# Optimization experiments

Hardware: AMD Instinct MI355X
Metric: run time of the kernel (lower is better)

## Reference

```python
import jax, jax.numpy as jnp
import numpy as np

I, O, R = 64, 64, 896          # input / output / regulatory protein counts
N = I + O + R                  # total GRN size
WARMUP = 25                    # warmup_count


def setup_inputs() -> dict:
    key = jax.random.key(0)
    k1, k2, k3, k4 = jax.random.split(key, 4)
    return {
        "inputs": jax.random.uniform(k1, (16384, I), dtype=jnp.float32),
        "identifiers": jax.random.uniform(k2, (N,), dtype=jnp.float32),
        "enhancers": jax.random.uniform(k3, (N,), dtype=jnp.float32),
        "inhibitors": jax.random.uniform(k4, (N,), dtype=jnp.float32),
        "beta": jnp.full((1,), 2.0, dtype=jnp.float32),
        "delta": jnp.full((1,), 1.0, dtype=jnp.float32),
    }


def _signatures(identifiers, enhancers, inhibitors, beta):
    # sig[j, i] = exp(-beta * |tag_j - id_i|): affinity of protein j regulating protein i.
    enh = jnp.exp(-beta * jnp.abs(enhancers[:, None] - identifiers[None, :]))
    inh = jnp.exp(-beta * jnp.abs(inhibitors[:, None] - identifiers[None, :]))
    # output proteins do not regulate others -> zero their rows
    mask = jnp.ones((N,), dtype=enh.dtype).at[I:I + O].set(0.0)[:, None]
    return enh * mask, inh * mask


def _step(conc, sig_diff, delta):
    # conc: [..., N]; sig_diff = enh_sigs - inh_sigs: [N, N]
    dc = (delta / N) * (conc @ sig_diff)
    new = jnp.maximum(conc + dc, 0.0)
    reg = new[..., I:]                                    # outputs + regulatory
    s = jnp.sum(reg, axis=-1, keepdims=True)
    reg = jnp.where(s > 0, reg / s, reg)                  # renormalize
    return jnp.concatenate([conc[..., :I], reg], axis=-1)  # inputs clamped


def reference(inputs, identifiers, enhancers, inhibitors, beta, delta):
    b, d = beta[0], delta[0]
    enh_s, inh_s = _signatures(identifiers, enhancers, inhibitors, b)
    sig_diff = enh_s - inh_s

    # setup(): uniform initial concentrations; warmup(): shared sequential steps
    conc0 = jnp.full((N,), 1.0 / N, dtype=jnp.float32)
    def warm(c, _):
        return _step(c, sig_diff, d), None
    conc, _ = jax.lax.scan(warm, conc0, None, length=WARMUP)

    # per-sample (batched instead of tf.map_fn): set input concs, one step
    B = inputs.shape[0]
    batch_conc = jnp.concatenate(
        [inputs, jnp.broadcast_to(conc[I:], (B, N - I))], axis=-1)
    new = _step(batch_conc, sig_diff, d)
    return new[..., I:I + O]  # output protein concentrations [B, O]
```

## Files before the change

kernel.cpp:

```cpp
#include <hip/hip_runtime.h>
#include <math.h>

#define NJ 960
#define NSRC 896
#define NWARM 25

typedef unsigned long long u64;
typedef unsigned int u32;

#define RK_O 0u
#define CT_O 896u
#define HD_O 1856u
#define BASE_F 8192u

#define TAG_RK 0x524B0001u
#define TAG_CT 0x43540001u
#define TAG_HD 0x48440001u

__device__ __forceinline__ void ast(u64* p, u64 v) {
  __hip_atomic_store(p, v, __ATOMIC_RELAXED, __HIP_MEMORY_SCOPE_AGENT);
}
__device__ __forceinline__ u64 ald(const u64* p) {
  return __hip_atomic_load(p, __ATOMIC_RELAXED, __HIP_MEMORY_SCOPE_AGENT);
}
__device__ __forceinline__ u32 poll32(const u64* p, u32 tag) {
  u64 v = ald(p);
  while ((u32)(v >> 32) != tag) { __builtin_amdgcn_s_sleep(1); v = ald(p); }
  return (u32)v;
}

__global__ __launch_bounds__(256) void front_k(const float* __restrict__ ident,
                                               const float* __restrict__ enh,
                                               const float* __restrict__ inh,
                                               const float* __restrict__ beta,
                                               const float* __restrict__ delta,
                                               void* __restrict__ wsv) {
  u64* RK = (u64*)wsv + RK_O;
  u64* CT = (u64*)wsv + CT_O;
  u64* HD = (u64*)wsv + HD_O;
  float* base = (float*)wsv + BASE_F;

  const int tid = threadIdx.x;
  const float bb = beta[0];
  const float dN = delta[0] / 1024.0f;

  if (blockIdx.x > 0) {
    const int g = (int)(blockIdx.x - 1) * 256 + tid;
    const int c8 = g & 7;
    if (g < NSRC * 8) {
      int m = g >> 3;
      float myE = enh[128 + m], myI = inh[128 + m];
      int re = 0, ri = 0;
      for (int i = 112 * c8; i < 112 * c8 + 112; ++i) {
        float ev = enh[128 + i], iv = inh[128 + i];
        re += (ev < myE || (ev == myE && i < m)) ? 1 : 0;
        ri += (iv < myI || (iv == myI && i < m)) ? 1 : 0;
      }
      int p = re | (ri << 16);
      p += __shfl_xor(p, 1); p += __shfl_xor(p, 2); p += __shfl_xor(p, 4);
      if (c8 == 0) ast(&RK[m], ((u64)TAG_RK << 32) | (u32)p);
    }
    {
      int j = g >> 3;
      float cj = ident[64 + j];
      int ce = 0, ci = 0;
      for (int i = 112 * c8; i < 112 * c8 + 112; ++i) {
        ce += (enh[128 + i] <= cj) ? 1 : 0;
        ci += (inh[128 + i] <= cj) ? 1 : 0;
      }
      int p = ce | (ci << 16);
      p += __shfl_xor(p, 1); p += __shfl_xor(p, 2); p += __shfl_xor(p, 4);
      if (c8 == 0) ast(&CT[j], ((u64)TAG_CT << 32) | (u32)p);
    }
    {
      int j = g >> 3;
      float cj = ident[64 + j];
      float h = 0.0f;
      for (int k = 8 * c8; k < 8 * c8 + 8; ++k)
        h += expf(-bb * fabsf(enh[k] - cj)) - expf(-bb * fabsf(inh[k] - cj));
      h += __shfl_xor(h, 1); h += __shfl_xor(h, 2); h += __shfl_xor(h, 4);
      if (c8 == 0)
        ast(&HD[j], ((u64)TAG_HD << 32) |
                    (u64)__float_as_uint(dN * h * (1.0f / 1024.0f)));
    }
    return;
  }

  __shared__ float yl[NJ];
  __shared__ float2 scanE[1024];
  __shared__ float2 scanI[1024];
  __shared__ float4 wtot[4];
  __shared__ float ssw[4];

  const int lane = tid & 63, wvid = tid >> 6;

  int rE[4], rI[4];
  if (tid < 224) {
    #pragma unroll
    for (int s = 0; s < 4; ++s) {
      u32 v = poll32(&RK[4 * tid + s], TAG_RK);
      rE[s] = v & 0xFFFF; rI[s] = v >> 16;
    }
  }
  int cE[4], cI[4];
  float hd[4], fm[4], fp[4];
  if (tid < 240) {
    #pragma unroll
    for (int c = 0; c < 4; ++c) {
      u32 v = poll32(&CT[4 * tid + c], TAG_CT);
      cE[c] = v & 0xFFFF; cI[c] = v >> 16;
      hd[c] = __uint_as_float(poll32(&HD[4 * tid + c], TAG_HD));
      float cj = ident[64 + 4 * tid + c];
      fm[c] = expf(-bb * cj); fp[c] = expf(bb * cj);
    }
  }
  float EP[4], EN[4], IP[4], IN2[4];
  if (tid < 224) {
    #pragma unroll
    for (int s = 0; s < 4; ++s) {
      float e = enh[128 + 4 * tid + s], i2 = inh[128 + 4 * tid + s];
      EP[s] = expf(bb * e);  EN[s] = expf(-bb * e);
      IP[s] = expf(bb * i2); IN2[s] = expf(-bb * i2);
    }
  }
  float y_own[4] = {1.0f / 1024.0f, 1.0f / 1024.0f, 1.0f / 1024.0f, 1.0f / 1024.0f};
  if (tid < 240) {
    #pragma unroll
    for (int c = 0; c < 4; ++c) yl[4 * tid + c] = 1.0f / 1024.0f;
  }
  __syncthreads();

  for (int t = 0; t <= NWARM; ++t) {
    if (tid == 0) {
      scanE[0] = make_float2(0.f, 0.f);
      scanI[0] = make_float2(0.f, 0.f);
    }
    if (tid >= 224) {
      #pragma unroll
      for (int c = 0; c < 4; ++c) {
        int p = 4 * tid + c;
        if (p > NSRC) {
          scanE[p] = make_float2(0.f, 0.f);
          scanI[p] = make_float2(0.f, 0.f);
        }
      }
    }
    if (tid < 224) {
      #pragma unroll
      for (int s = 0; s < 4; ++s) {
        float ym = yl[64 + 4 * tid + s];
        scanE[rE[s] + 1] = make_float2(ym * EP[s], ym * EN[s]);
        scanI[rI[s] + 1] = make_float2(ym * IP[s], ym * IN2[s]);
      }
    }
    __syncthreads();

    float2 e0 = scanE[4 * tid], e1 = scanE[4 * tid + 1],
           e2 = scanE[4 * tid + 2], e3 = scanE[4 * tid + 3];
    float2 i0 = scanI[4 * tid], i1 = scanI[4 * tid + 1],
           i2v = scanI[4 * tid + 2], i3 = scanI[4 * tid + 3];
    e1.x += e0.x; e1.y += e0.y; e2.x += e1.x; e2.y += e1.y; e3.x += e2.x; e3.y += e2.y;
    i1.x += i0.x; i1.y += i0.y; i2v.x += i1.x; i2v.y += i1.y; i3.x += i2v.x; i3.y += i2v.y;
    float4 tot = make_float4(e3.x, e3.y, i3.x, i3.y);
    float4 inc = tot;
    #pragma unroll
    for (int off = 1; off < 64; off <<= 1) {
      float ox = __shfl_up(inc.x, off, 64);
      float oy = __shfl_up(inc.y, off, 64);
      float oz = __shfl_up(inc.z, off, 64);
      float ow = __shfl_up(inc.w, off, 64);
      if (lane >= off) { inc.x += ox; inc.y += oy; inc.z += oz; inc.w += ow; }
    }
    if (lane == 63) wtot[wvid] = inc;
    __syncthreads();
    float4 exc = make_float4(inc.x - tot.x, inc.y - tot.y,
                             inc.z - tot.z, inc.w - tot.w);
    #pragma unroll
    for (int w = 0; w < 3; ++w)
      if (w < wvid) {
        float4 p = wtot[w];
        exc.x += p.x; exc.y += p.y; exc.z += p.z; exc.w += p.w;
      }
    e0.x += exc.x; e0.y += exc.y; e1.x += exc.x; e1.y += exc.y;
    e2.x += exc.x; e2.y += exc.y; e3.x += exc.x; e3.y += exc.y;
    i0.x += exc.z; i0.y += exc.w; i1.x += exc.z; i1.y += exc.w;
    i2v.x += exc.z; i2v.y += exc.w; i3.x += exc.z; i3.y += exc.w;
    scanE[4 * tid] = e0; scanE[4 * tid + 1] = e1;
    scanE[4 * tid + 2] = e2; scanE[4 * tid + 3] = e3;
    scanI[4 * tid] = i0; scanI[4 * tid + 1] = i1;
    scanI[4 * tid + 2] = i2v; scanI[4 * tid + 3] = i3;
    __syncthreads();

    float nv[4] = {0.f, 0.f, 0.f, 0.f};
    float psum = 0.0f;
    if (tid < 240) {
      float2 TE = scanE[NSRC], TI = scanI[NSRC];
      #pragma unroll
      for (int c = 0; c < 4; ++c) {
        float2 AE = scanE[cE[c]], AI = scanI[cI[c]];
        float dot = fm[c] * AE.x + fp[c] * (TE.y - AE.y)
                  - fm[c] * AI.x - fp[c] * (TI.y - AI.y);
        float pre = y_own[c] + dN * dot;
        if (t < NWARM) {
          nv[c] = fmaxf(pre + hd[c], 0.0f);
          psum += nv[c];
        } else {
          base[4 * tid + c] = pre;
        }
      }
    }
    if (t < NWARM) {
      #pragma unroll
      for (int off = 32; off >= 1; off >>= 1) psum += __shfl_xor(psum, off);
      if (lane == 0) ssw[wvid] = psum;
      __syncthreads();
      float s = ssw[0] + ssw[1] + ssw[2] + ssw[3];
      float inv = (s > 0.0f) ? 1.0f / s : 1.0f;
      if (tid < 240) {
        #pragma unroll
        for (int c = 0; c < 4; ++c) {
          y_own[c] = nv[c] * inv;
          yl[4 * tid + c] = y_own[c];
        }
      }
    }
    __syncthreads();
  }
}

__global__ __launch_bounds__(512) void batch_k(const float* __restrict__ inp,
                                               const float* __restrict__ ident,
                                               const float* __restrict__ enh,
                                               const float* __restrict__ inh,
                                               const float* __restrict__ beta,
                                               const float* __restrict__ delta,
                                               const float* __restrict__ ws,
                                               float* __restrict__ out) {
  __shared__ float At[64][66];
  __shared__ float Wl[16][512];
  __shared__ float bch[NJ];
  __shared__ float4 Ek4[64];
  __shared__ float2 Ei2[64];

  const int tid = threadIdx.x;
  const int colg = tid & 63;
  const int rowg = tid >> 6;
  const size_t rowbase = (size_t)blockIdx.x * 64;
  const float bb = beta[0];
  const float dN = delta[0] / 1024.0f;

  #pragma unroll
  for (int i = 0; i < 2; ++i) {
    int fi = tid + i * 512;
    int r = fi >> 4, c4 = (fi & 15) * 4;
    float4 f4 = *(const float4*)(inp + (rowbase + r) * 64 + c4);
    At[c4 + 0][r] = f4.x; At[c4 + 1][r] = f4.y;
    At[c4 + 2][r] = f4.z; At[c4 + 3][r] = f4.w;
  }
  if (tid < 64) {
    float e = enh[tid], iv = inh[tid];
    Ek4[tid] = make_float4(expf(bb * e), expf(-bb * e),
                           expf(bb * iv), expf(-bb * iv));
    Ei2[tid] = make_float2(e, iv);
  }
  if (tid < 240) {
    float4 b4 = *(const float4*)(ws + BASE_F + 4 * tid);
    bch[4 * tid + 0] = b4.x; bch[4 * tid + 1] = b4.y;
    bch[4 * tid + 2] = b4.z; bch[4 * tid + 3] = b4.w;
  }

  float acc[8][8];
  float rs[8];
  #pragma unroll
  for (int r = 0; r < 8; ++r) rs[r] = 0.0f;

  #pragma unroll 1
  for (int ch = 0; ch < 2; ++ch) {
    const int c0 = ch ? 0 : 512;
    const bool ok = (c0 + tid) < NJ;
    const float cj = ok ? ident[64 + c0 + tid] : 0.0f;
    const float fpc = expf(bb * cj), fmc = expf(-bb * cj);

    #pragma unroll
    for (int r = 0; r < 8; ++r)
      #pragma unroll
      for (int c = 0; c < 8; ++c) acc[r][c] = 0.0f;

    #pragma unroll 1
    for (int s = 0; s < 4; ++s) {
      __syncthreads();
      #pragma unroll 4
      for (int e = 0; e < 16; ++e) {
        int k = 16 * s + e;
        float4 E = Ek4[k];
        float2 ei = Ei2[k];
        float w = 0.0f;
        if (ok)
          w = dN * (((ei.x >= cj) ? E.y * fpc : E.x * fmc)
                  - ((ei.y >= cj) ? E.w * fpc : E.z * fmc));
        Wl[e][tid] = w;
      }
      __syncthreads();
      #pragma unroll
      for (int kk = 0; kk < 16; ++kk) {
        float4 a0 = *(const float4*)&At[16 * s + kk][rowg * 8];
        float4 a1 = *(const float4*)&At[16 * s + kk][rowg * 8 + 4];
        float4 w0 = *(const float4*)&Wl[kk][colg * 4];
        float4 w1 = *(const float4*)&Wl[kk][256 + colg * 4];
        float a_[8] = {a0.x, a0.y, a0.z, a0.w, a1.x, a1.y, a1.z, a1.w};
        float w_[8] = {w0.x, w0.y, w0.z, w0.w, w1.x, w1.y, w1.z, w1.w};
        #pragma unroll
        for (int r = 0; r < 8; ++r)
          #pragma unroll
          for (int c = 0; c < 8; ++c)
            acc[r][c] = fmaf(a_[r], w_[c], acc[r][c]);
      }
    }

    #pragma unroll
    for (int c = 0; c < 8; ++c) {
      int cl = (c < 4) ? (colg * 4 + c) : (256 + colg * 4 + (c - 4));
      int j = c0 + cl;
      float bv = (j < NJ) ? bch[j] : -1.0e30f;
      #pragma unroll
      for (int r = 0; r < 8; ++r)
        rs[r] += fmaxf(acc[r][c] + bv, 0.0f);
    }
  }

  #pragma unroll
  for (int r = 0; r < 8; ++r) {
    float v = rs[r];
    #pragma unroll
    for (int off = 32; off >= 1; off >>= 1) v += __shfl_xor(v, off);
    rs[r] = v;
  }
  if (colg < 16) {
    #pragma unroll
    for (int r = 0; r < 8; ++r) {
      float inv = (rs[r] > 0.0f) ? 1.0f / rs[r] : 1.0f;
      float* op = out + (rowbase + rowg * 8 + r) * 64 + colg * 4;
      float4 o;
      o.x = fmaxf(acc[r][0] + bch[colg * 4 + 0], 0.0f) * inv;
      o.y = fmaxf(acc[r][1] + bch[colg * 4 + 1], 0.0f) * inv;
      o.z = fmaxf(acc[r][2] + bch[colg * 4 + 2], 0.0f) * inv;
      o.w = fmaxf(acc[r][3] + bch[colg * 4 + 3], 0.0f) * inv;
      *(float4*)op = o;
    }
  }
}

extern "C" void kernel_launch(void* const* d_in, const int* in_sizes, int n_in,
                              void* d_out, int out_size, void* d_ws, size_t ws_size,
                              hipStream_t stream) {
  const float* inp   = (const float*)d_in[0];
  const float* ident = (const float*)d_in[1];
  const float* enh   = (const float*)d_in[2];
  const float* inh   = (const float*)d_in[3];
  const float* beta  = (const float*)d_in[4];
  const float* delta = (const float*)d_in[5];

  hipLaunchKernelGGL(front_k, dim3(31), dim3(256), 0, stream,
                     ident, enh, inh, beta, delta, d_ws);
  hipLaunchKernelGGL(batch_k, dim3(256), dim3(512), 0, stream,
                     inp, ident, enh, inh, beta, delta,
                     (const float*)d_ws, (float*)d_out);
}
```

Baseline: 160.8 us.

## Precompute input-row weight matrix in front kernel and halve batch tile rows

The 64x960 input-to-node weight block is now computed once by 30 extra blocks in the front kernel and stored in the workspace. The batch kernel streams these weights from global memory instead of recomputing exponentials per block. The batch tile also shrinks from 64 to 32 rows, which doubles the grid to 512 blocks for better occupancy and CU coverage. In exchange, each block has a lower FMA-to-load ratio and extra global weight traffic, which L2 should mostly serve.

```diff
diff --git a/kernel.cpp b/kernel.cpp
--- a/kernel.cpp
+++ b/kernel.cpp
@@ -11,7 +11,8 @@
 #define RK_O 0u
 #define CT_O 896u
 #define HD_O 1856u
-#define BASE_F 8192u
+#define WK_F 8192u
+#define BASE_F 69632u
 
 #define TAG_RK 0x524B0001u
 #define TAG_CT 0x43540001u
@@ -38,11 +39,26 @@
   u64* RK = (u64*)wsv + RK_O;
   u64* CT = (u64*)wsv + CT_O;
   u64* HD = (u64*)wsv + HD_O;
+  float* Wk = (float*)wsv + WK_F;
   float* base = (float*)wsv + BASE_F;
 
   const int tid = threadIdx.x;
   const float bb = beta[0];
   const float dN = delta[0] / 1024.0f;
+
+  if (blockIdx.x > 30) {
+    const int g2 = (int)(blockIdx.x - 31) * 256 + tid;
+    int k = g2 / 120;
+    int jb = (g2 % 120) * 8;
+    float ek = enh[k], ik = inh[k];
+    #pragma unroll
+    for (int u = 0; u < 8; ++u) {
+      float cj = ident[64 + jb + u];
+      Wk[(size_t)k * NJ + jb + u] =
+          dN * (expf(-bb * fabsf(ek - cj)) - expf(-bb * fabsf(ik - cj)));
+    }
+    return;
+  }
 
   if (blockIdx.x > 0) {
     const int g = (int)(blockIdx.x - 1) * 256 + tid;
@@ -229,39 +245,23 @@
 }
 
 __global__ __launch_bounds__(512) void batch_k(const float* __restrict__ inp,
-                                               const float* __restrict__ ident,
-                                               const float* __restrict__ enh,
-                                               const float* __restrict__ inh,
-                                               const float* __restrict__ beta,
-                                               const float* __restrict__ delta,
                                                const float* __restrict__ ws,
                                                float* __restrict__ out) {
-  __shared__ float At[64][66];
+  __shared__ float At[64][36];
   __shared__ float Wl[16][512];
   __shared__ float bch[NJ];
-  __shared__ float4 Ek4[64];
-  __shared__ float2 Ei2[64];
 
   const int tid = threadIdx.x;
   const int colg = tid & 63;
   const int rowg = tid >> 6;
-  const size_t rowbase = (size_t)blockIdx.x * 64;
-  const float bb = beta[0];
-  const float dN = delta[0] / 1024.0f;
-
-  #pragma unroll
-  for (int i = 0; i < 2; ++i) {
-    int fi = tid + i * 512;
-    int r = fi >> 4, c4 = (fi & 15) * 4;
+  const size_t rowbase = (size_t)blockIdx.x * 32;
+  const float* __restrict__ Wk = ws + WK_F;
+
+  {
+    int r = tid >> 4, c4 = (tid & 15) * 4;
     float4 f4 = *(const float4*)(inp + (rowbase + r) * 64 + c4);
     At[c4 + 0][r] = f4.x; At[c4 + 1][r] = f4.y;
     At[c4 + 2][r] = f4.z; At[c4 + 3][r] = f4.w;
-  }
-  if (tid < 64) {
-    float e = enh[tid], iv = inh[tid];
-    Ek4[tid] = make_float4(expf(bb * e), expf(-bb * e),
-                           expf(bb * iv), expf(-bb * iv));
-    Ei2[tid] = make_float2(e, iv);
   }
   if (tid < 240) {
     float4 b4 = *(const float4*)(ws + BASE_F + 4 * tid);
@@ -269,48 +269,42 @@
     bch[4 * tid + 2] = b4.z; bch[4 * tid + 3] = b4.w;
   }
 
-  float acc[8][8];
-  float rs[8];
-  #pragma unroll
-  for (int r = 0; r < 8; ++r) rs[r] = 0.0f;
+  float acc[4][8];
+  float rs[4] = {0.f, 0.f, 0.f, 0.f};
 
   #pragma unroll 1
   for (int ch = 0; ch < 2; ++ch) {
     const int c0 = ch ? 0 : 512;
-    const bool ok = (c0 + tid) < NJ;
-    const float cj = ok ? ident[64 + c0 + tid] : 0.0f;
-    const float fpc = expf(bb * cj), fmc = expf(-bb * cj);
-
-    #pragma unroll
-    for (int r = 0; r < 8; ++r)
+
+    #pragma unroll
+    for (int r = 0; r < 4; ++r)
       #pragma unroll
       for (int c = 0; c < 8; ++c) acc[r][c] = 0.0f;
 
     #pragma unroll 1
     for (int s = 0; s < 4; ++s) {
       __syncthreads();
-      #pragma unroll 4
-      for (int e = 0; e < 16; ++e) {
-        int k = 16 * s + e;
-        float4 E = Ek4[k];
-        float2 ei = Ei2[k];
-        float w = 0.0f;
-        if (ok)
-          w = dN * (((ei.x >= cj) ? E.y * fpc : E.x * fmc)
-                  - ((ei.y >= cj) ? E.w * fpc : E.z * fmc));
-        Wl[e][tid] = w;
+      #pragma unroll
+      for (int i = 0; i < 4; ++i) {
+        int fi = tid + i * 512;
+        int kk = fi >> 7;
+        int c4 = (fi & 127) * 4;
+        int j = c0 + c4;
+        float4 v = make_float4(0.f, 0.f, 0.f, 0.f);
+        if (j < NJ)
+          v = *(const float4*)(Wk + (size_t)(16 * s + kk) * NJ + j);
+        *(float4*)&Wl[kk][c4] = v;
       }
       __syncthreads();
       #pragma unroll
       for (int kk = 0; kk < 16; ++kk) {
-        float4 a0 = *(const float4*)&At[16 * s + kk][rowg * 8];
-        float4 a1 = *(const float4*)&At[16 * s + kk][rowg * 8 + 4];
+        float4 av = *(const float4*)&At[16 * s + kk][rowg * 4];
         float4 w0 = *(const float4*)&Wl[kk][colg * 4];
         float4 w1 = *(const float4*)&Wl[kk][256 + colg * 4];
-        float a_[8] = {a0.x, a0.y, a0.z, a0.w, a1.x, a1.y, a1.z, a1.w};
+        float a_[4] = {av.x, av.y, av.z, av.w};
         float w_[8] = {w0.x, w0.y, w0.z, w0.w, w1.x, w1.y, w1.z, w1.w};
         #pragma unroll
-        for (int r = 0; r < 8; ++r)
+        for (int r = 0; r < 4; ++r)
           #pragma unroll
           for (int c = 0; c < 8; ++c)
             acc[r][c] = fmaf(a_[r], w_[c], acc[r][c]);
@@ -323,13 +317,13 @@
       int j = c0 + cl;
       float bv = (j < NJ) ? bch[j] : -1.0e30f;
       #pragma unroll
-      for (int r = 0; r < 8; ++r)
+      for (int r = 0; r < 4; ++r)
         rs[r] += fmaxf(acc[r][c] + bv, 0.0f);
     }
   }
 
   #pragma unroll
-  for (int r = 0; r < 8; ++r) {
+  for (int r = 0; r < 4; ++r) {
     float v = rs[r];
     #pragma unroll
     for (int off = 32; off >= 1; off >>= 1) v += __shfl_xor(v, off);
@@ -337,9 +331,9 @@
   }
   if (colg < 16) {
     #pragma unroll
-    for (int r = 0; r < 8; ++r) {
+    for (int r = 0; r < 4; ++r) {
       float inv = (rs[r] > 0.0f) ? 1.0f / rs[r] : 1.0f;
-      float* op = out + (rowbase + rowg * 8 + r) * 64 + colg * 4;
+      float* op = out + (rowbase + rowg * 4 + r) * 64 + colg * 4;
       float4 o;
       o.x = fmaxf(acc[r][0] + bch[colg * 4 + 0], 0.0f) * inv;
       o.y = fmaxf(acc[r][1] + bch[colg * 4 + 1], 0.0f) * inv;
@@ -360,9 +354,8 @@
   const float* beta  = (const float*)d_in[4];
   const float* delta = (const float*)d_in[5];
 
-  hipLaunchKernelGGL(front_k, dim3(31), dim3(256), 0, stream,
+  hipLaunchKernelGGL(front_k, dim3(61), dim3(256), 0, stream,
                      ident, enh, inh, beta, delta, d_ws);
-  hipLaunchKernelGGL(batch_k, dim3(256), dim3(512), 0, stream,
-                     inp, ident, enh, inh, beta, delta,
-                     (const float*)d_ws, (float*)d_out);
-}
+  hipLaunchKernelGGL(batch_k, dim3(512), dim3(512), 0, stream,
+                     inp, (const float*)d_ws, (float*)d_out);
+}
```

Measured after the change: 155.1 us. -3.6%, faster.

## Fuse warmup and batch kernels, overlapping per-block warmup scan with GEMM

Applied to the files above, without the earlier changes.

Merges the two-kernel pipeline into one 576-thread kernel. Every block redundantly runs the 25-step warmup recurrence in a dedicated high-priority wave using a single-wave scan, while 8 other waves compute the batch GEMM chunks that do not need the warmup bias. An LDS flag signals when the bias is ready, and the first chunk is computed after that. This removes the second launch and the global round trip for the bias, at the cost of redundant warmup work in all 256 blocks and inter-block polling on the tagged counters.

```diff
diff --git a/kernel.cpp b/kernel.cpp
--- a/kernel.cpp
+++ b/kernel.cpp
@@ -11,7 +11,6 @@
 #define RK_O 0u
 #define CT_O 896u
 #define HD_O 1856u
-#define BASE_F 8192u
 
 #define TAG_RK 0x524B0001u
 #define TAG_CT 0x43540001u
@@ -25,27 +24,58 @@
 }
 __device__ __forceinline__ u32 poll32(const u64* p, u32 tag) {
   u64 v = ald(p);
-  while ((u32)(v >> 32) != tag) { __builtin_amdgcn_s_sleep(1); v = ald(p); }
+  while ((u32)(v >> 32) != tag) { __builtin_amdgcn_s_sleep(8); v = ald(p); }
   return (u32)v;
 }
 
-__global__ __launch_bounds__(256) void front_k(const float* __restrict__ ident,
-                                               const float* __restrict__ enh,
-                                               const float* __restrict__ inh,
-                                               const float* __restrict__ beta,
-                                               const float* __restrict__ delta,
-                                               void* __restrict__ wsv) {
+__global__ __launch_bounds__(576) void grn_one(
+    const float* __restrict__ inp, const float* __restrict__ ident,
+    const float* __restrict__ enh, const float* __restrict__ inh,
+    const float* __restrict__ beta, const float* __restrict__ delta,
+    void* __restrict__ wsv, float* __restrict__ out) {
+  __shared__ float2 SE[16][64];
+  __shared__ float2 SI[16][64];
+  __shared__ float4 SRCX[NSRC];
+  __shared__ float4 HEK[64];
+  __shared__ float2 HEI[64];
+  __shared__ float At[64][68];
+  __shared__ float bch[NJ];
+  __shared__ u32 sflag;
+
   u64* RK = (u64*)wsv + RK_O;
   u64* CT = (u64*)wsv + CT_O;
   u64* HD = (u64*)wsv + HD_O;
-  float* base = (float*)wsv + BASE_F;
 
   const int tid = threadIdx.x;
   const float bb = beta[0];
   const float dN = delta[0] / 1024.0f;
-
-  if (blockIdx.x > 0) {
-    const int g = (int)(blockIdx.x - 1) * 256 + tid;
+  const size_t rowbase = (size_t)blockIdx.x * 64;
+
+  #pragma unroll
+  for (int it = 0; it < 2; ++it) {
+    int fi = tid + it * 576;
+    if (fi < 1024) {
+      int r = fi >> 4, c4 = (fi & 15) * 4;
+      float4 f4 = *(const float4*)(inp + (rowbase + r) * 64 + c4);
+      At[c4 + 0][r] = f4.x; At[c4 + 1][r] = f4.y;
+      At[c4 + 2][r] = f4.z; At[c4 + 3][r] = f4.w;
+    }
+  }
+  for (int m = tid; m < NSRC; m += 576) {
+    float e = enh[128 + m], iv = inh[128 + m];
+    SRCX[m] = make_float4(expf(bb * e), expf(-bb * e),
+                          expf(bb * iv), expf(-bb * iv));
+  }
+  if (tid < 64) {
+    float e = enh[tid], iv = inh[tid];
+    HEK[tid] = make_float4(expf(bb * e), expf(-bb * e),
+                           expf(bb * iv), expf(-bb * iv));
+    HEI[tid] = make_float2(e, iv);
+  }
+  if (tid == 0) sflag = 0;
+
+  if (blockIdx.x < 30 && tid < 256) {
+    const int g = (int)blockIdx.x * 256 + tid;
     const int c8 = g & 7;
     if (g < NSRC * 8) {
       int m = g >> 3;
@@ -83,250 +113,186 @@
         ast(&HD[j], ((u64)TAG_HD << 32) |
                     (u64)__float_as_uint(dN * h * (1.0f / 1024.0f)));
     }
+  }
+  __syncthreads();
+
+  if (tid >= 512) {
+    __builtin_amdgcn_s_setprio(1);
+    const int lane = tid - 512;
+    const int c0l = lane * 15;
+
+    #pragma unroll
+    for (int u = 0; u < 16; ++u) {
+      SE[u][lane] = make_float2(0.f, 0.f);
+      SI[u][lane] = make_float2(0.f, 0.f);
+    }
+
+    float fmv[15], fpv[15], hdv[15], y[15];
+    int cc[15], rr[15];
+    #pragma unroll
+    for (int s = 0; s < 15; ++s) {
+      float cj = ident[64 + c0l + s];
+      fmv[s] = expf(-bb * cj); fpv[s] = expf(bb * cj);
+      y[s] = 1.0f / 1024.0f;
+      rr[s] = 0;
+    }
+    #pragma unroll
+    for (int s = 0; s < 15; ++s) {
+      cc[s] = (int)poll32(&CT[c0l + s], TAG_CT);
+      hdv[s] = __uint_as_float(poll32(&HD[c0l + s], TAG_HD));
+    }
+    #pragma unroll
+    for (int s = 0; s < 15; ++s) {
+      int c = c0l + s;
+      if (c >= 64) rr[s] = (int)poll32(&RK[c - 64], TAG_RK);
+    }
+
+    for (int t = 0; t <= NWARM; ++t) {
+      #pragma unroll
+      for (int s = 0; s < 15; ++s) {
+        int c = c0l + s;
+        if (c >= 64) {
+          float4 X = SRCX[c - 64];
+          int qE = (rr[s] & 0xFFFF) + 1;
+          int qI = ((rr[s] >> 16) & 0xFFFF) + 1;
+          SE[qE & 15][qE >> 4] = make_float2(y[s] * X.x, y[s] * X.y);
+          SI[qI & 15][qI >> 4] = make_float2(y[s] * X.z, y[s] * X.w);
+        }
+      }
+      asm volatile("s_waitcnt lgkmcnt(0)" ::: "memory");
+      __builtin_amdgcn_sched_barrier(0);
+
+      float2 tE = make_float2(0.f, 0.f), tI = make_float2(0.f, 0.f);
+      #pragma unroll
+      for (int u = 0; u < 16; ++u) {
+        float2 a = SE[u][lane], b = SI[u][lane];
+        tE.x += a.x; tE.y += a.y; tI.x += b.x; tI.y += b.y;
+      }
+      float4 inc = make_float4(tE.x, tE.y, tI.x, tI.y);
+      float4 tot = inc;
+      #pragma unroll
+      for (int off = 1; off < 64; off <<= 1) {
+        float ox = __shfl_up(inc.x, off, 64);
+        float oy = __shfl_up(inc.y, off, 64);
+        float oz = __shfl_up(inc.z, off, 64);
+        float ow = __shfl_up(inc.w, off, 64);
+        if (lane >= off) { inc.x += ox; inc.y += oy; inc.z += oz; inc.w += ow; }
+      }
+      float TEy = __shfl(inc.y, 63, 64);
+      float TIy = __shfl(inc.w, 63, 64);
+      float2 pe = make_float2(inc.x - tot.x, inc.y - tot.y);
+      float2 pi = make_float2(inc.z - tot.z, inc.w - tot.w);
+
+      #pragma unroll
+      for (int u = 0; u < 16; ++u) {
+        float2 a = SE[u][lane], b = SI[u][lane];
+        pe.x += a.x; pe.y += a.y; pi.x += b.x; pi.y += b.y;
+        if (lane * 16 + u <= NSRC) { SE[u][lane] = pe; SI[u][lane] = pi; }
+      }
+      asm volatile("s_waitcnt lgkmcnt(0)" ::: "memory");
+      __builtin_amdgcn_sched_barrier(0);
+
+      float nv[15]; float psum = 0.0f;
+      #pragma unroll
+      for (int s = 0; s < 15; ++s) {
+        int cE = cc[s] & 0xFFFF, cI = (cc[s] >> 16) & 0xFFFF;
+        float2 AE = SE[cE & 15][cE >> 4];
+        float2 AI = SI[cI & 15][cI >> 4];
+        float dot = fmv[s] * AE.x + fpv[s] * (TEy - AE.y)
+                  - fmv[s] * AI.x - fpv[s] * (TIy - AI.y);
+        float pre = y[s] + dN * dot;
+        if (t < NWARM) {
+          nv[s] = fmaxf(pre + hdv[s], 0.0f);
+          psum += nv[s];
+        } else {
+          bch[c0l + s] = pre;
+        }
+      }
+      if (t < NWARM) {
+        #pragma unroll
+        for (int off = 32; off >= 1; off >>= 1) psum += __shfl_xor(psum, off);
+        float invs = (psum > 0.0f) ? 1.0f / psum : 1.0f;
+        #pragma unroll
+        for (int s = 0; s < 15; ++s) y[s] = nv[s] * invs;
+      }
+    }
+    asm volatile("s_waitcnt lgkmcnt(0)" ::: "memory");
+    __hip_atomic_store(&sflag, 1u, __ATOMIC_RELEASE,
+                       __HIP_MEMORY_SCOPE_WORKGROUP);
+    __builtin_amdgcn_s_setprio(0);
     return;
   }
 
-  __shared__ float yl[NJ];
-  __shared__ float2 scanE[1024];
-  __shared__ float2 scanI[1024];
-  __shared__ float4 wtot[4];
-  __shared__ float ssw[4];
-
-  const int lane = tid & 63, wvid = tid >> 6;
-
-  int rE[4], rI[4];
-  if (tid < 224) {
-    #pragma unroll
-    for (int s = 0; s < 4; ++s) {
-      u32 v = poll32(&RK[4 * tid + s], TAG_RK);
-      rE[s] = v & 0xFFFF; rI[s] = v >> 16;
-    }
-  }
-  int cE[4], cI[4];
-  float hd[4], fm[4], fp[4];
-  if (tid < 240) {
-    #pragma unroll
-    for (int c = 0; c < 4; ++c) {
-      u32 v = poll32(&CT[4 * tid + c], TAG_CT);
-      cE[c] = v & 0xFFFF; cI[c] = v >> 16;
-      hd[c] = __uint_as_float(poll32(&HD[4 * tid + c], TAG_HD));
-      float cj = ident[64 + 4 * tid + c];
-      fm[c] = expf(-bb * cj); fp[c] = expf(bb * cj);
-    }
-  }
-  float EP[4], EN[4], IP[4], IN2[4];
-  if (tid < 224) {
-    #pragma unroll
-    for (int s = 0; s < 4; ++s) {
-      float e = enh[128 + 4 * tid + s], i2 = inh[128 + 4 * tid + s];
-      EP[s] = expf(bb * e);  EN[s] = expf(-bb * e);
-      IP[s] = expf(bb * i2); IN2[s] = expf(-bb * i2);
-    }
-  }
-  float y_own[4] = {1.0f / 1024.0f, 1.0f / 1024.0f, 1.0f / 1024.0f, 1.0f / 1024.0f};
-  if (tid < 240) {
-    #pragma unroll
-    for (int c = 0; c < 4; ++c) yl[4 * tid + c] = 1.0f / 1024.0f;
-  }
-  __syncthreads();
-
-  for (int t = 0; t <= NWARM; ++t) {
-    if (tid == 0) {
-      scanE[0] = make_float2(0.f, 0.f);
-      scanI[0] = make_float2(0.f, 0.f);
-    }
-    if (tid >= 224) {
-      #pragma unroll
-      for (int c = 0; c < 4; ++c) {
-        int p = 4 * tid + c;
-        if (p > NSRC) {
-          scanE[p] = make_float2(0.f, 0.f);
-          scanI[p] = make_float2(0.f, 0.f);
-        }
-      }
-    }
-    if (tid < 224) {
-      #pragma unroll
-      for (int s = 0; s < 4; ++s) {
-        float ym = yl[64 + 4 * tid + s];
-        scanE[rE[s] + 1] = make_float2(ym * EP[s], ym * EN[s]);
-        scanI[rI[s] + 1] = make_float2(ym * IP[s], ym * IN2[s]);
-      }
-    }
-    __syncthreads();
-
-    float2 e0 = scanE[4 * tid], e1 = scanE[4 * tid + 1],
-           e2 = scanE[4 * tid + 2], e3 = scanE[4 * tid + 3];
-    float2 i0 = scanI[4 * tid], i1 = scanI[4 * tid + 1],
-           i2v = scanI[4 * tid + 2], i3 = scanI[4 * tid + 3];
-    e1.x += e0.x; e1.y += e0.y; e2.x += e1.x; e2.y += e1.y; e3.x += e2.x; e3.y += e2.y;
-    i1.x += i0.x; i1.y += i0.y; i2v.x += i1.x; i2v.y += i1.y; i3.x += i2v.x; i3.y += i2v.y;
-    float4 tot = make_float4(e3.x, e3.y, i3.x, i3.y);
-    float4 inc = tot;
-    #pragma unroll
-    for (int off = 1; off < 64; off <<= 1) {
-      float ox = __shfl_up(inc.x, off, 64);
-      float oy = __shfl_up(inc.y, off, 64);
-      float oz = __shfl_up(inc.z, off, 64);
-      float ow = __shfl_up(inc.w, off, 64);
-      if (lane >= off) { inc.x += ox; inc.y += oy; inc.z += oz; inc.w += ow; }
-    }
-    if (lane == 63) wtot[wvid] = inc;
-    __syncthreads();
-    float4 exc = make_float4(inc.x - tot.x, inc.y - tot.y,
-                             inc.z - tot.z, inc.w - tot.w);
-    #pragma unroll
-    for (int w = 0; w < 3; ++w)
-      if (w < wvid) {
-        float4 p = wtot[w];
-        exc.x += p.x; exc.y += p.y; exc.z += p.z; exc.w += p.w;
-      }
-    e0.x += exc.x; e0.y += exc.y; e1.x += exc.x; e1.y += exc.y;
-    e2.x += exc.x; e2.y += exc.y; e3.x += exc.x; e3.y += exc.y;
-    i0.x += exc.z; i0.y += exc.w; i1.x += exc.z; i1.y += exc.w;
-    i2v.x += exc.z; i2v.y += exc.w; i3.x += exc.z; i3.y += exc.w;
-    scanE[4 * tid] = e0; scanE[4 * tid + 1] = e1;
-    scanE[4 * tid + 2] = e2; scanE[4 * tid + 3] = e3;
-    scanI[4 * tid] = i0; scanI[4 * tid + 1] = i1;
-    scanI[4 * tid + 2] = i2v; scanI[4 * tid + 3] = i3;
-    __syncthreads();
-
-    float nv[4] = {0.f, 0.f, 0.f, 0.f};
-    float psum = 0.0f;
-    if (tid < 240) {
-      float2 TE = scanE[NSRC], TI = scanI[NSRC];
-      #pragma unroll
-      for (int c = 0; c < 4; ++c) {
-        float2 AE = scanE[cE[c]], AI = scanI[cI[c]];
-        float dot = fm[c] * AE.x + fp[c] * (TE.y - AE.y)
-                  - fm[c] * AI.x - fp[c] * (TI.y - AI.y);
-        float pre = y_own[c] + dN * dot;
-        if (t < NWARM) {
-          nv[c] = fmaxf(pre + hd[c], 0.0f);
-          psum += nv[c];
-        } else {
-          base[4 * tid + c] = pre;
-        }
-      }
-    }
-    if (t < NWARM) {
-      #pragma unroll
-      for (int off = 32; off >= 1; off >>= 1) psum += __shfl_xor(psum, off);
-      if (lane == 0) ssw[wvid] = psum;
-      __syncthreads();
-      float s = ssw[0] + ssw[1] + ssw[2] + ssw[3];
-      float inv = (s > 0.0f) ? 1.0f / s : 1.0f;
-      if (tid < 240) {
-        #pragma unroll
-        for (int c = 0; c < 4; ++c) {
-          y_own[c] = nv[c] * inv;
-          yl[4 * tid + c] = y_own[c];
-        }
-      }
-    }
-    __syncthreads();
-  }
-}
-
-__global__ __launch_bounds__(512) void batch_k(const float* __restrict__ inp,
-                                               const float* __restrict__ ident,
-                                               const float* __restrict__ enh,
-                                               const float* __restrict__ inh,
-                                               const float* __restrict__ beta,
-                                               const float* __restrict__ delta,
-                                               const float* __restrict__ ws,
-                                               float* __restrict__ out) {
-  __shared__ float At[64][66];
-  __shared__ float Wl[16][512];
-  __shared__ float bch[NJ];
-  __shared__ float4 Ek4[64];
-  __shared__ float2 Ei2[64];
-
-  const int tid = threadIdx.x;
-  const int colg = tid & 63;
-  const int rowg = tid >> 6;
-  const size_t rowbase = (size_t)blockIdx.x * 64;
-  const float bb = beta[0];
-  const float dN = delta[0] / 1024.0f;
-
-  #pragma unroll
-  for (int i = 0; i < 2; ++i) {
-    int fi = tid + i * 512;
-    int r = fi >> 4, c4 = (fi & 15) * 4;
-    float4 f4 = *(const float4*)(inp + (rowbase + r) * 64 + c4);
-    At[c4 + 0][r] = f4.x; At[c4 + 1][r] = f4.y;
-    At[c4 + 2][r] = f4.z; At[c4 + 3][r] = f4.w;
-  }
-  if (tid < 64) {
-    float e = enh[tid], iv = inh[tid];
-    Ek4[tid] = make_float4(expf(bb * e), expf(-bb * e),
-                           expf(bb * iv), expf(-bb * iv));
-    Ei2[tid] = make_float2(e, iv);
-  }
-  if (tid < 240) {
-    float4 b4 = *(const float4*)(ws + BASE_F + 4 * tid);
-    bch[4 * tid + 0] = b4.x; bch[4 * tid + 1] = b4.y;
-    bch[4 * tid + 2] = b4.z; bch[4 * tid + 3] = b4.w;
-  }
-
-  float acc[8][8];
+  const int lane = tid & 63;
+  const int wv = tid >> 6;
+  const int rw = wv * 8;
+
   float rs[8];
   #pragma unroll
   for (int r = 0; r < 8; ++r) rs[r] = 0.0f;
 
-  #pragma unroll 1
-  for (int ch = 0; ch < 2; ++ch) {
-    const int c0 = ch ? 0 : 512;
-    const bool ok = (c0 + tid) < NJ;
-    const float cj = ok ? ident[64 + c0 + tid] : 0.0f;
-    const float fpc = expf(bb * cj), fmc = expf(-bb * cj);
-
+  float acc0[8][4], acc1[8][4], acc2[8][4], acc3[8][4];
+
+  auto run_chunk = [&](int c0, float (&acc)[8][4]) {
+    float cjv[4], fpd[4], fmd[4];
+    #pragma unroll
+    for (int u = 0; u < 4; ++u) {
+      int j = c0 + lane * 4 + u;
+      bool okj = j < NJ;
+      float cj = okj ? ident[64 + j] : 0.0f;
+      cjv[u] = cj;
+      fpd[u] = okj ? dN * expf(bb * cj) : 0.0f;
+      fmd[u] = okj ? dN * expf(-bb * cj) : 0.0f;
+    }
     #pragma unroll
     for (int r = 0; r < 8; ++r)
       #pragma unroll
-      for (int c = 0; c < 8; ++c) acc[r][c] = 0.0f;
-
-    #pragma unroll 1
-    for (int s = 0; s < 4; ++s) {
-      __syncthreads();
-      #pragma unroll 4
-      for (int e = 0; e < 16; ++e) {
-        int k = 16 * s + e;
-        float4 E = Ek4[k];
-        float2 ei = Ei2[k];
-        float w = 0.0f;
-        if (ok)
-          w = dN * (((ei.x >= cj) ? E.y * fpc : E.x * fmc)
-                  - ((ei.y >= cj) ? E.w * fpc : E.z * fmc));
-        Wl[e][tid] = w;
-      }
-      __syncthreads();
-      #pragma unroll
-      for (int kk = 0; kk < 16; ++kk) {
-        float4 a0 = *(const float4*)&At[16 * s + kk][rowg * 8];
-        float4 a1 = *(const float4*)&At[16 * s + kk][rowg * 8 + 4];
-        float4 w0 = *(const float4*)&Wl[kk][colg * 4];
-        float4 w1 = *(const float4*)&Wl[kk][256 + colg * 4];
-        float a_[8] = {a0.x, a0.y, a0.z, a0.w, a1.x, a1.y, a1.z, a1.w};
-        float w_[8] = {w0.x, w0.y, w0.z, w0.w, w1.x, w1.y, w1.z, w1.w};
+      for (int u = 0; u < 4; ++u) acc[r][u] = 0.0f;
+    #pragma unroll 4
+    for (int kk = 0; kk < 64; ++kk) {
+      float2 ei = HEI[kk];
+      float4 E = HEK[kk];
+      float w[4];
+      #pragma unroll
+      for (int u = 0; u < 4; ++u) {
+        float we = (ei.x >= cjv[u]) ? E.y * fpd[u] : E.x * fmd[u];
+        float wi = (ei.y >= cjv[u]) ? E.w * fpd[u] : E.z * fmd[u];
+        w[u] = we - wi;
+      }
+      float4 a0 = *(const float4*)&At[kk][rw];
+      float4 a1 = *(const float4*)&At[kk][rw + 4];
+      float a_[8] = {a0.x, a0.y, a0.z, a0.w, a1.x, a1.y, a1.z, a1.w};
+      #pragma unroll
+      for (int r = 0; r < 8; ++r)
         #pragma unroll
-        for (int r = 0; r < 8; ++r)
-          #pragma unroll
-          for (int c = 0; c < 8; ++c)
-            acc[r][c] = fmaf(a_[r], w_[c], acc[r][c]);
-      }
-    }
-
-    #pragma unroll
-    for (int c = 0; c < 8; ++c) {
-      int cl = (c < 4) ? (colg * 4 + c) : (256 + colg * 4 + (c - 4));
-      int j = c0 + cl;
+        for (int u = 0; u < 4; ++u)
+          acc[r][u] = fmaf(a_[r], w[u], acc[r][u]);
+    }
+  };
+  auto fold_chunk = [&](int c0, float (&acc)[8][4]) {
+    #pragma unroll
+    for (int u = 0; u < 4; ++u) {
+      int j = c0 + lane * 4 + u;
       float bv = (j < NJ) ? bch[j] : -1.0e30f;
       #pragma unroll
       for (int r = 0; r < 8; ++r)
-        rs[r] += fmaxf(acc[r][c] + bv, 0.0f);
-    }
-  }
+        rs[r] += fmaxf(acc[r][u] + bv, 0.0f);
+    }
+  };
+
+  run_chunk(256, acc1);
+  run_chunk(512, acc2);
+  run_chunk(768, acc3);
+
+  while (__hip_atomic_load(&sflag, __ATOMIC_ACQUIRE,
+                           __HIP_MEMORY_SCOPE_WORKGROUP) == 0u)
+    __builtin_amdgcn_s_sleep(16);
+
+  fold_chunk(256, acc1);
+  fold_chunk(512, acc2);
+  fold_chunk(768, acc3);
+  run_chunk(0, acc0);
+  fold_chunk(0, acc0);
 
   #pragma unroll
   for (int r = 0; r < 8; ++r) {
@@ -335,16 +301,16 @@
     for (int off = 32; off >= 1; off >>= 1) v += __shfl_xor(v, off);
     rs[r] = v;
   }
-  if (colg < 16) {
+  if (lane < 16) {
     #pragma unroll
     for (int r = 0; r < 8; ++r) {
       float inv = (rs[r] > 0.0f) ? 1.0f / rs[r] : 1.0f;
-      float* op = out + (rowbase + rowg * 8 + r) * 64 + colg * 4;
+      float* op = out + (rowbase + rw + r) * 64 + lane * 4;
       float4 o;
-      o.x = fmaxf(acc[r][0] + bch[colg * 4 + 0], 0.0f) * inv;
-      o.y = fmaxf(acc[r][1] + bch[colg * 4 + 1], 0.0f) * inv;
-      o.z = fmaxf(acc[r][2] + bch[colg * 4 + 2], 0.0f) * inv;
-      o.w = fmaxf(acc[r][3] + bch[colg * 4 + 3], 0.0f) * inv;
+      o.x = fmaxf(acc0[r][0] + bch[lane * 4 + 0], 0.0f) * inv;
+      o.y = fmaxf(acc0[r][1] + bch[lane * 4 + 1], 0.0f) * inv;
+      o.z = fmaxf(acc0[r][2] + bch[lane * 4 + 2], 0.0f) * inv;
+      o.w = fmaxf(acc0[r][3] + bch[lane * 4 + 3], 0.0f) * inv;
       *(float4*)op = o;
     }
   }
@@ -360,9 +326,6 @@
   const float* beta  = (const float*)d_in[4];
   const float* delta = (const float*)d_in[5];
 
-  hipLaunchKernelGGL(front_k, dim3(31), dim3(256), 0, stream,
-                     ident, enh, inh, beta, delta, d_ws);
-  hipLaunchKernelGGL(batch_k, dim3(256), dim3(512), 0, stream,
-                     inp, ident, enh, inh, beta, delta,
-                     (const float*)d_ws, (float*)d_out);
-}
+  hipLaunchKernelGGL(grn_one, dim3(256), dim3(576), 0, stream,
+                     inp, ident, enh, inh, beta, delta, d_ws, (float*)d_out);
+}
```

New measurement: 207.6 us. 29.1% more time.
